# Kernel optimization log

Hardware: AMD Instinct MI355X
Metric: run time of the kernel (lower is better)

## Reference

```python
import jax, jax.numpy as jnp
import numpy as np

BETA_MAX = 0.995
BETA_MIN = 0.05
EPI_AGE_PENALTY = 0.02
EPI_STRENGTH_BOOST = 0.5
EPI_STRENGTH_DECAY = 0.995
EPI_WRITE_ALPHA = 0.5
EVICT_AGE_BOOST = 0.05
EVICT_STR_PENALTY = 0.5
SLOT_TEMP = 50.0
SWITCH_TAU = 0.5

B, H, K, U, OBS, SSUM, PROJ = 2048, 256, 32, 128, 128, 128, 128


def setup_inputs() -> dict:
    key = jax.random.key(0)
    ks = jax.random.split(key, 20)
    def gl(k, shape, fan_in):
        return jax.random.normal(k, shape, jnp.float32) / np.sqrt(fan_in).astype(np.float32)
    inp = {}
    inp['h_prev'] = jax.random.normal(ks[0], (B, H), jnp.float32)
    inp['keys'] = jax.random.normal(ks[1], (B, K, H), jnp.float32)
    inp['vals'] = jax.random.normal(ks[2], (B, K, H), jnp.float32)
    inp['age'] = jax.random.uniform(ks[3], (B, K), jnp.float32) * 100.0
    inp['strength'] = jax.random.uniform(ks[4], (B, K), jnp.float32)
    inp['obs'] = jax.random.normal(ks[5], (B, OBS), jnp.float32)
    inp['ssum'] = jax.random.normal(ks[6], (B, SSUM), jnp.float32)
    inp['u_int_prev'] = jax.random.normal(ks[7], (B, U), jnp.float32)
    inp['step_in_macro'] = jax.random.randint(ks[8], (B,), 0, 4, jnp.int32)
    # learned parameters
    inp['W_obs'] = gl(ks[9], (OBS, PROJ), OBS); inp['b_obs'] = jnp.zeros((PROJ,), jnp.float32)
    inp['W_ssum'] = gl(ks[10], (SSUM, PROJ), SSUM); inp['b_ssum'] = jnp.zeros((PROJ,), jnp.float32)
    XIN = 2 * PROJ
    inp['Wi'] = gl(ks[11], (XIN, 3 * H), XIN); inp['bi'] = jnp.zeros((3 * H,), jnp.float32)
    inp['Wh'] = gl(ks[12], (H, 3 * H), H); inp['bhn'] = jnp.zeros((H,), jnp.float32)
    inp['W_gate'] = gl(ks[13], (H, 1), H); inp['b_gate'] = jnp.zeros((1,), jnp.float32)
    inp['W_mean'] = gl(ks[14], (2 * H, U), 2 * H); inp['b_mean'] = jnp.zeros((U,), jnp.float32)
    inp['u_logstd'] = jnp.full((U,), -1.0, jnp.float32)
    inp['W_beta'] = gl(ks[15], (2 * H, 1), 2 * H); inp['b_beta'] = jnp.zeros((1,), jnp.float32)
    inp['W_sw'] = gl(ks[16], (2 * H, 1), 2 * H); inp['b_sw'] = jnp.zeros((1,), jnp.float32)
    return inp


def reference(h_prev, keys, vals, age, strength, obs, ssum, u_int_prev, step_in_macro,
              W_obs, b_obs, W_ssum, b_ssum, Wi, bi, Wh, bhn, W_gate, b_gate,
              W_mean, b_mean, u_logstd, W_beta, b_beta, W_sw, b_sw):
    Kslots = keys.shape[1]
    # input projections + GRU step (flax GRUCell: h' = (1-z)*n + z*h)
    xo = jnp.tanh(obs @ W_obs + b_obs)
    xs = jnp.tanh(ssum @ W_ssum + b_ssum)
    x_in = jnp.concatenate([xo, xs], axis=-1)
    gi = x_in @ Wi + bi
    gh = h_prev @ Wh
    ir, iz, inn = jnp.split(gi, 3, axis=-1)
    hr, hz, hn = jnp.split(gh, 3, axis=-1)
    r = jax.nn.sigmoid(ir + hr)
    z = jax.nn.sigmoid(iz + hz)
    n = jnp.tanh(inn + r * (hn + bhn))
    h_t = (1.0 - z) * n + z * h_prev
    # write gate
    w_str = jax.nn.sigmoid(h_t @ W_gate + b_gate)  # [B,1]
    # episodic slot memory: cosine-sim read
    qn = h_t / (jnp.linalg.norm(h_t, axis=-1, keepdims=True) + 1e-6)
    kn = keys / (jnp.linalg.norm(keys, axis=-1, keepdims=True) + 1e-6)
    sim_r = jnp.einsum('bkd,bd->bk', kn, qn)
    logits = sim_r + EPI_STRENGTH_BOOST * jnp.log(jnp.clip(strength, 1e-3, 1.0)) - EPI_AGE_PENALTY * age
    w_read = jax.nn.softmax(logits, axis=-1)
    read_out = jnp.einsum('bk,bkd->bd', w_read, vals)
    # write addressing (write_vec == query_vec == h_t so sim_w == sim_r)
    wk_n = qn
    sim_w = sim_r
    evict = EVICT_AGE_BOOST * jnp.log1p(age) - EVICT_STR_PENALTY * strength
    write_soft = jax.nn.softmax(sim_w * SLOT_TEMP + evict, axis=-1)
    write_hard = jax.nn.one_hot(jnp.argmax(write_soft, axis=-1), Kslots, dtype=jnp.float32)
    write_w = jax.lax.stop_gradient(write_hard - write_soft) + write_soft  # straight-through
    ws = jnp.clip(w_str, 0.0, 1.0)  # [B,1]
    eff_rate = write_w * ws * EPI_WRITE_ALPHA  # [B,K]
    rate = eff_rate[:, :, None]
    keys_new = (1.0 - rate) * keys + rate * wk_n[:, None, :]
    vals_new = (1.0 - rate) * vals + rate * h_t[:, None, :]
    age_new = (age + 1.0) * (1.0 - write_w)
    str_new = strength * EPI_STRENGTH_DECAY
    str_new = jnp.clip(str_new + write_w * ws * (1.0 - str_new), 0.0, 1.0)
    # heads
    ctx = jnp.concatenate([h_t, read_out], axis=-1)
    mean = ctx @ W_mean + b_mean
    beta = BETA_MIN + (BETA_MAX - BETA_MIN) * jax.nn.sigmoid((ctx @ W_beta + b_beta)[:, 0])
    sw_prob = jax.nn.sigmoid((ctx @ W_sw + b_sw)[:, 0])
    # deterministic path (rng=None): u_prop = mean, threshold switch
    u_prop = mean
    switch_f = jnp.where(sw_prob > SWITCH_TAU, 1.0, 0.0)
    is_boundary = jnp.where(step_in_macro == 0, 1.0, 0.0)
    switch_f = jnp.maximum(switch_f, is_boundary)
    sw_f = switch_f[:, None]
    beta_eff = beta[:, None] * (1.0 - sw_f)
    u_int = beta_eff * u_int_prev + (1.0 - beta_eff) * u_prop
    return (h_t, keys_new, vals_new, age_new, str_new, u_prop,
            switch_f.astype(jnp.int32), u_int, beta, sw_prob)
```

## Files before the change

kernel.cpp:

```cpp
#include <hip/hip_runtime.h>
#include <math.h>

#define Bdim 2048
#define Hdim 256
#define KS 32
#define Udim 128
#define OBSD 128
#define PROJD 128
#define H3 768

__device__ __forceinline__ float sigm(float x){ return 1.0f/(1.0f+__expf(-x)); }

typedef float __attribute__((ext_vector_type(4))) f32x4;

__device__ __forceinline__ float4 ntload4(const float* p){
    f32x4 v = __builtin_nontemporal_load((const f32x4*)p);
    return make_float4(v.x, v.y, v.z, v.w);
}
__device__ __forceinline__ void ntstore4(float* p, float4 q){
    f32x4 v = {q.x, q.y, q.z, q.w};
    __builtin_nontemporal_store(v, (f32x4*)p);
}

__global__ __launch_bounds__(256) void kA1(
    const float* __restrict__ obs, const float* __restrict__ ssum,
    const float* __restrict__ W_obs, const float* __restrict__ b_obs,
    const float* __restrict__ W_ssum, const float* __restrict__ b_ssum,
    float* __restrict__ xin)
{
    __shared__ float s_in[2][8][128];
    const int t = threadIdx.x;
    const int r0 = blockIdx.x * 8;

    {
        int r = t >> 5, c4 = (t & 31) << 2;
        float4 v = *(const float4*)(obs + (size_t)(r0+r)*OBSD + c4);
        s_in[0][r][c4+0]=v.x; s_in[0][r][c4+1]=v.y; s_in[0][r][c4+2]=v.z; s_in[0][r][c4+3]=v.w;
        v = *(const float4*)(ssum + (size_t)(r0+r)*OBSD + c4);
        s_in[1][r][c4+0]=v.x; s_in[1][r][c4+1]=v.y; s_in[1][r][c4+2]=v.z; s_in[1][r][c4+3]=v.w;
    }
    __syncthreads();

    const int col = t & 127;
    const int src = t >> 7;
    const float* Wp = src ? W_ssum : W_obs;
    const float bb = src ? b_ssum[col] : b_obs[col];

    float acc[8] = {0,0,0,0,0,0,0,0};
    for (int i=0;i<128;i++){
        float w = Wp[i*PROJD + col];
        #pragma unroll
        for (int r=0;r<8;r++) acc[r] = fmaf(s_in[src][r][i], w, acc[r]);
    }
    #pragma unroll
    for (int r=0;r<8;r++)
        xin[(size_t)(r0+r)*256 + t] = tanhf(acc[r] + bb);
}

__global__ __launch_bounds__(256) void kG2(
    const float* __restrict__ xin, const float* __restrict__ hp,
    const float* __restrict__ Wi, const float* __restrict__ Wh,
    float* __restrict__ g)
{
    __shared__ float Xt[2][16][68];
    __shared__ float Wt[2][16][64];

    const int t = threadIdx.x;
    const int bx = blockIdx.x >> 4;
    const int by = blockIdx.x & 15;
    const int r0 = bx * 64;
    const int c0 = by * 64;

    const int kbeg = (c0 >= 768) ? 256 : 0;
    const int kend = (c0 >= 512 && c0 < 768) ? 256 : 512;
    const int nck  = (kend - kbeg) >> 4;

    const int sr  = t >> 2;
    const int sk4 = (t & 3) << 2;
    const size_t xbase = (size_t)(r0 + sr) * 256 + sk4;
    const int wk  = t >> 4;
    const int wc4 = (t & 15) << 2;
    const int cW  = (c0 < 512) ? c0 : (c0 - 256);

    const int rowA = (t & 15) << 2;
    const int colA = (t >> 4) << 2;

    float acc[4][4] = {{0.f}};
    float4 xr, wr;

    {
        const int k0 = kbeg;
        const float* xs = (k0 < 256) ? (xin + xbase + k0) : (hp + xbase + (k0 - 256));
        xr = *(const float4*)xs;
        const int k = k0 + wk;
        const float* wsrc = (k < 256) ? (Wi + (size_t)k*H3 + c0 + wc4)
                                      : (Wh + (size_t)(k-256)*H3 + cW + wc4);
        wr = *(const float4*)wsrc;
    }
    Xt[0][sk4+0][sr] = xr.x; Xt[0][sk4+1][sr] = xr.y;
    Xt[0][sk4+2][sr] = xr.z; Xt[0][sk4+3][sr] = xr.w;
    *(float4*)&Wt[0][wk][wc4] = wr;
    __syncthreads();

    for (int ck = 0; ck < nck; ck++){
        const int cur = ck & 1;
        const bool more = (ck + 1 < nck);
        if (more){
            const int k0 = kbeg + ((ck + 1) << 4);
            const float* xs = (k0 < 256) ? (xin + xbase + k0) : (hp + xbase + (k0 - 256));
            xr = *(const float4*)xs;
            const int k = k0 + wk;
            const float* wsrc = (k < 256) ? (Wi + (size_t)k*H3 + c0 + wc4)
                                          : (Wh + (size_t)(k-256)*H3 + cW + wc4);
            wr = *(const float4*)wsrc;
        }
        #pragma unroll
        for (int kk = 0; kk < 16; kk++){
            float4 a4 = *(const float4*)&Xt[cur][kk][rowA];
            float4 b4 = *(const float4*)&Wt[cur][kk][colA];
            float av[4] = {a4.x, a4.y, a4.z, a4.w};
            float bv[4] = {b4.x, b4.y, b4.z, b4.w};
            #pragma unroll
            for (int i=0;i<4;i++)
                #pragma unroll
                for (int j=0;j<4;j++)
                    acc[i][j] = fmaf(av[i], bv[j], acc[i][j]);
        }
        if (more){
            const int nxt = cur ^ 1;
            Xt[nxt][sk4+0][sr] = xr.x; Xt[nxt][sk4+1][sr] = xr.y;
            Xt[nxt][sk4+2][sr] = xr.z; Xt[nxt][sk4+3][sr] = xr.w;
            *(float4*)&Wt[nxt][wk][wc4] = wr;
            __syncthreads();
        }
    }

    #pragma unroll
    for (int i=0;i<4;i++){
        float4 o = make_float4(acc[i][0], acc[i][1], acc[i][2], acc[i][3]);
        *(float4*)&g[(size_t)(r0 + rowA + i)*1024 + c0 + colA] = o;
    }
}

__global__ __launch_bounds__(256) void kA3(
    const float* __restrict__ g, const float* __restrict__ h_prev,
    const float* __restrict__ bi, const float* __restrict__ bhn,
    const float* __restrict__ W_gate, const float* __restrict__ b_gate,
    float* __restrict__ out_h, float* __restrict__ ws_qn, float* __restrict__ ws_wstr)
{
    __shared__ float redA[8][4], redB[8][4];
    __shared__ float s_inv[8];
    const int t = threadIdx.x;
    const int r0 = blockIdx.x * 8;

    const float bir = bi[t], biz = bi[t+256], bin_ = bi[t+512];
    const float bh = bhn[t];
    const float wg = W_gate[t];
    const int lane = t & 63, wid = t >> 6;

    float hv[8];
    #pragma unroll
    for (int r=0;r<8;r++){
        const size_t gb = (size_t)(r0+r)*1024;
        float gr = g[gb + t];
        float gz = g[gb + 256 + t];
        float gni = g[gb + 512 + t];
        float gnh = g[gb + 768 + t];
        float hp = h_prev[(size_t)(r0+r)*Hdim + t];
        float rr = sigm(gr + bir);
        float zz = sigm(gz + biz);
        float nn = tanhf(gni + bin_ + rr*(gnh + bh));
        hv[r] = (1.0f - zz)*nn + zz*hp;
    }

    #pragma unroll
    for (int r=0;r<8;r++){
        float a = hv[r]*hv[r];
        float b2 = hv[r]*wg;
        #pragma unroll
        for (int off=32; off>=1; off>>=1){
            a  += __shfl_down(a, off);
            b2 += __shfl_down(b2, off);
        }
        if (lane==0){ redA[r][wid]=a; redB[r][wid]=b2; }
    }
    __syncthreads();
    if (t < 8){
        float ss = redA[t][0]+redA[t][1]+redA[t][2]+redA[t][3];
        float gd = redB[t][0]+redB[t][1]+redB[t][2]+redB[t][3];
        s_inv[t] = 1.0f/(sqrtf(ss) + 1e-6f);
        ws_wstr[r0+t] = sigm(gd + b_gate[0]);
    }
    __syncthreads();
    #pragma unroll
    for (int r=0;r<8;r++){
        out_h[(size_t)(r0+r)*Hdim + t] = hv[r];
        ws_qn[(size_t)(r0+r)*Hdim + t] = hv[r]*s_inv[r];
    }
}

__global__ __launch_bounds__(256) void kB(
    const float* __restrict__ keys, const float* __restrict__ vals,
    const float* __restrict__ age, const float* __restrict__ strength,
    const float* __restrict__ h_t, const float* __restrict__ ws_qn,
    const float* __restrict__ ws_wstr,
    float* __restrict__ keys_new, float* __restrict__ vals_new,
    float* __restrict__ age_new, float* __restrict__ str_new,
    float* __restrict__ ws_ro)
{
    __shared__ float s_sim[KS], s_wr[KS], s_rate[KS];
    __shared__ float4 s_ro[4][64];

    const int b = blockIdx.x;
    const int t = threadIdx.x, lane = t & 63, wid = t >> 6;

    float ag = 0.f, st = 0.f, wstr = 0.f;
    if (t < KS){
        ag = age[b*KS+t];
        st = strength[b*KS+t];
        wstr = ws_wstr[b];
    }

    const float4 q4 = ((const float4*)(ws_qn + (size_t)b*Hdim))[lane];
    const float4 h4 = ((const float4*)(h_t  + (size_t)b*Hdim))[lane];

    const float* Kb = keys + (size_t)b*KS*Hdim;
    const float* Vb = vals + (size_t)b*KS*Hdim;
    float4 kreg[8], vreg[8];
    float v[16];
    #pragma unroll
    for (int s=0;s<8;s++){
        const int k = wid*8 + s;
        kreg[s] = ntload4(Kb + k*Hdim + lane*4);
        vreg[s] = ntload4(Vb + k*Hdim + lane*4);
        v[2*s]   = kreg[s].x*q4.x + kreg[s].y*q4.y + kreg[s].z*q4.z + kreg[s].w*q4.w;
        v[2*s+1] = kreg[s].x*kreg[s].x + kreg[s].y*kreg[s].y + kreg[s].z*kreg[s].z + kreg[s].w*kreg[s].w;
    }

    {
        const bool hb5 = (lane & 32) != 0;
        #pragma unroll
        for (int i=0;i<8;i++){
            float send = hb5 ? v[i] : v[i+8];
            float recv = __shfl_xor(send, 32);
            v[i] = (hb5 ? v[i+8] : v[i]) + recv;
        }
        const bool hb4 = (lane & 16) != 0;
        #pragma unroll
        for (int i=0;i<4;i++){
            float send = hb4 ? v[i] : v[i+4];
            float recv = __shfl_xor(send, 16);
            v[i] = (hb4 ? v[i+4] : v[i]) + recv;
        }
        const bool hb3 = (lane & 8) != 0;
        #pragma unroll
        for (int i=0;i<2;i++){
            float send = hb3 ? v[i] : v[i+2];
            float recv = __shfl_xor(send, 8);
            v[i] = (hb3 ? v[i+2] : v[i]) + recv;
        }
        const bool hb2 = (lane & 4) != 0;
        {
            float send = hb2 ? v[0] : v[1];
            float recv = __shfl_xor(send, 4);
            v[0] = (hb2 ? v[1] : v[0]) + recv;
        }
        float r0 = v[0];
        r0 += __shfl_xor(r0, 2);
        r0 += __shfl_xor(r0, 1);
        float other = __shfl_xor(r0, 4);
        if ((lane & 7) == 0){
            s_sim[wid*8 + (lane>>3)] = r0 / (sqrtf(other) + 1e-6f);
        }
    }
    __syncthreads();

    if (t < KS){
        float sim = s_sim[t];
        float cl = fminf(fmaxf(st, 0.001f), 1.0f);
        float logit = sim + 0.5f*logf(cl) - 0.02f*ag;
        float wl = 50.0f*sim + 0.05f*log1pf(ag) - 0.5f*st;

        float lmax = logit;
        #pragma unroll
        for (int off=16; off>=1; off>>=1)
            lmax = fmaxf(lmax, __shfl_xor(lmax, off));
        float e = __expf(logit - lmax);
        float es = e;
        #pragma unroll
        for (int off=16; off>=1; off>>=1)
            es += __shfl_xor(es, off);

        float wm = wl; int ki = t;
        #pragma unroll
        for (int off=16; off>=1; off>>=1){
            float ow = __shfl_xor(wm, off);
            int   ok = __shfl_xor(ki, off);
            if (ow > wm || (ow == wm && ok < ki)){ wm = ow; ki = ok; }
        }

        s_wr[t] = e / es;
        float hard = (t == ki) ? 1.0f : 0.0f;
        s_rate[t] = hard * 0.5f * wstr;
        age_new[b*KS+t] = (ag + 1.0f)*(1.0f - hard);
        float sd = st*0.995f;
        float sn = sd + hard*wstr*(1.0f - sd);
        str_new[b*KS+t] = fminf(fmaxf(sn,0.f),1.f);
    }
    __syncthreads();

    float4 ro = make_float4(0.f,0.f,0.f,0.f);
    float* KNb = keys_new + (size_t)b*KS*Hdim;
    float* VNb = vals_new + (size_t)b*KS*Hdim;
    #pragma unroll
    for (int s=0;s<8;s++){
        const int k = wid*8 + s;
        const float wr = s_wr[k];
        const float rate = s_rate[k];
        const float om = 1.0f - rate;
        ro.x = fmaf(wr, vreg[s].x, ro.x);
        ro.y = fmaf(wr, vreg[s].y, ro.y);
        ro.z = fmaf(wr, vreg[s].z, ro.z);
        ro.w = fmaf(wr, vreg[s].w, ro.w);
        float4 kn, vn;
        kn.x = om*kreg[s].x + rate*q4.x;
        kn.y = om*kreg[s].y + rate*q4.y;
        kn.z = om*kreg[s].z + rate*q4.z;
        kn.w = om*kreg[s].w + rate*q4.w;
        vn.x = om*vreg[s].x + rate*h4.x;
        vn.y = om*vreg[s].y + rate*h4.y;
        vn.z = om*vreg[s].z + rate*h4.z;
        vn.w = om*vreg[s].w + rate*h4.w;
        ntstore4(KNb + k*Hdim + lane*4, kn);
        ntstore4(VNb + k*Hdim + lane*4, vn);
    }
    s_ro[wid][lane] = ro;
    __syncthreads();
    if (t < 64){
        float4 a = s_ro[0][t], bb = s_ro[1][t], c = s_ro[2][t], d = s_ro[3][t];
        float4 r;
        r.x = a.x+bb.x+c.x+d.x;
        r.y = a.y+bb.y+c.y+d.y;
        r.z = a.z+bb.z+c.z+d.z;
        r.w = a.w+bb.w+c.w+d.w;
        ((float4*)(ws_ro + (size_t)b*Hdim))[t] = r;
    }
}

__global__ __launch_bounds__(256) void kC(
    const float* __restrict__ h_t, const float* __restrict__ ws_ro,
    const float* __restrict__ u_int_prev, const int* __restrict__ step_in_macro,
    const float* __restrict__ W_mean, const float* __restrict__ b_mean,
    const float* __restrict__ W_beta, const float* __restrict__ b_beta,
    const float* __restrict__ W_sw, const float* __restrict__ b_sw,
    float* __restrict__ out_uprop, float* __restrict__ out_switch,
    float* __restrict__ out_uint, float* __restrict__ out_beta, float* __restrict__ out_swp)
{
    __shared__ float s_ctx[4][512];
    __shared__ float redb[4][4], reds[4][4];
    __shared__ float s_beff[4];
    const int t = threadIdx.x;
    const int r0 = blockIdx.x * 4;

    {
        int r = t >> 6, c4 = (t & 63) << 2;
        float4 v = *(const float4*)(h_t + (size_t)(r0+r)*Hdim + c4);
        s_ctx[r][c4+0]=v.x; s_ctx[r][c4+1]=v.y; s_ctx[r][c4+2]=v.z; s_ctx[r][c4+3]=v.w;
        v = *(const float4*)(ws_ro + (size_t)(r0+r)*Hdim + c4);
        s_ctx[r][256+c4+0]=v.x; s_ctx[r][256+c4+1]=v.y; s_ctx[r][256+c4+2]=v.z; s_ctx[r][256+c4+3]=v.w;
    }
    __syncthreads();

    const int c = t & 127;
    const int rh = t >> 7;
    float acc[2] = {0.f, 0.f};
    for (int i=0;i<512;i++){
        float w = W_mean[i*Udim + c];
        acc[0] = fmaf(s_ctx[2*rh+0][i], w, acc[0]);
        acc[1] = fmaf(s_ctx[2*rh+1][i], w, acc[1]);
    }

    float pb[4]={0,0,0,0}, ps[4]={0,0,0,0};
    for (int i=t; i<512; i+=256){
        float wb = W_beta[i], wsw = W_sw[i];
        #pragma unroll
        for (int r=0;r<4;r++){
            pb[r] = fmaf(s_ctx[r][i], wb, pb[r]);
            ps[r] = fmaf(s_ctx[r][i], wsw, ps[r]);
        }
    }
    const int lane = t & 63, wid = t >> 6;
    #pragma unroll
    for (int r=0;r<4;r++){
        float a = pb[r], b2 = ps[r];
        #pragma unroll
        for (int off=32; off>=1; off>>=1){
            a  += __shfl_down(a, off);
            b2 += __shfl_down(b2, off);
        }
        if (lane==0){ redb[r][wid]=a; reds[r][wid]=b2; }
    }
    __syncthreads();
    if (t < 4){
        float db  = redb[t][0]+redb[t][1]+redb[t][2]+redb[t][3] + b_beta[0];
        float dsw = reds[t][0]+reds[t][1]+reds[t][2]+reds[t][3] + b_sw[0];
        float beta = 0.05f + 0.945f*sigm(db);
        float swp = sigm(dsw);
        float swf = (swp > 0.5f) ? 1.0f : 0.0f;
        if (step_in_macro[r0+t] == 0) swf = 1.0f;
        out_beta[r0+t] = beta;
        out_swp[r0+t] = swp;
        out_switch[r0+t] = swf;
        s_beff[t] = beta*(1.0f - swf);
    }
    __syncthreads();
    #pragma unroll
    for (int j=0;j<2;j++){
        int r = 2*rh + j;
        float mean = acc[j] + b_mean[c];
        size_t o = (size_t)(r0+r)*Udim + c;
        out_uprop[o] = mean;
        float be = s_beff[r];
        out_uint[o] = be*u_int_prev[o] + (1.0f-be)*mean;
    }
}

extern "C" void kernel_launch(void* const* d_in, const int* in_sizes, int n_in,
                              void* d_out, int out_size, void* d_ws, size_t ws_size,
                              hipStream_t stream)
{
    const float* h_prev   = (const float*)d_in[0];
    const float* keys     = (const float*)d_in[1];
    const float* vals     = (const float*)d_in[2];
    const float* age      = (const float*)d_in[3];
    const float* strength = (const float*)d_in[4];
    const float* obs      = (const float*)d_in[5];
    const float* ssum     = (const float*)d_in[6];
    const float* u_int_prev = (const float*)d_in[7];
    const int*   step     = (const int*)d_in[8];
    const float* W_obs    = (const float*)d_in[9];
    const float* b_obs    = (const float*)d_in[10];
    const float* W_ssum   = (const float*)d_in[11];
    const float* b_ssum   = (const float*)d_in[12];
    const float* Wi       = (const float*)d_in[13];
    const float* bi       = (const float*)d_in[14];
    const float* Wh       = (const float*)d_in[15];
    const float* bhn      = (const float*)d_in[16];
    const float* W_gate   = (const float*)d_in[17];
    const float* b_gate   = (const float*)d_in[18];
    const float* W_mean   = (const float*)d_in[19];
    const float* b_mean   = (const float*)d_in[20];
    const float* W_beta   = (const float*)d_in[22];
    const float* b_beta   = (const float*)d_in[23];
    const float* W_sw     = (const float*)d_in[24];
    const float* b_sw     = (const float*)d_in[25];

    float* out = (float*)d_out;
    float* out_h    = out;
    float* out_kn   = out_h   + 524288;
    float* out_vn   = out_kn  + 16777216;
    float* out_age  = out_vn  + 16777216;
    float* out_str  = out_age + 65536;
    float* out_up   = out_str + 65536;
    float* out_sw   = out_up  + 262144;
    float* out_ui   = out_sw  + 2048;
    float* out_beta = out_ui  + 262144;
    float* out_swp  = out_beta+ 2048;

    float* ws = (float*)d_ws;
    float* ws_qn   = ws;
    float* ws_ro   = ws + Bdim*Hdim;
    float* ws_wstr = ws + 2*Bdim*Hdim;

    float* ws_xin = out_vn;
    float* ws_g   = out_kn;

    kA1<<<Bdim/8, 256, 0, stream>>>(obs, ssum, W_obs, b_obs, W_ssum, b_ssum, ws_xin);
    kG2<<<512, 256, 0, stream>>>(ws_xin, h_prev, Wi, Wh, ws_g);
    kA3<<<Bdim/8, 256, 0, stream>>>(ws_g, h_prev, bi, bhn, W_gate, b_gate,
                                    out_h, ws_qn, ws_wstr);
    kB<<<Bdim, 256, 0, stream>>>(keys, vals, age, strength, out_h, ws_qn, ws_wstr,
                                 out_kn, out_vn, out_age, out_str, ws_ro);
    kC<<<Bdim/4, 256, 0, stream>>>(out_h, ws_ro, u_int_prev, step, W_mean, b_mean,
                                   W_beta, b_beta, W_sw, b_sw,
                                   out_up, out_sw, out_ui, out_beta, out_swp);
}
```

Measured before the change: 126.9 us.

## Split episodic memory kernel into similarity pass and update pass

The fused memory kernel is split into two kernels. The first reads keys and computes the read weights, the write rates, age and strength. The second rereads keys and vals to produce the read-out and write keys_new and vals_new. The aim is to cut register pressure from holding 16 float4 registers across the barrier and to raise occupancy. The cost is a second 64MB read of keys, which now uses cached rather than nontemporal loads in the hope that it hits the L2 or MALL cache, plus one extra kernel launch.

```diff
diff --git a/kernel.cpp b/kernel.cpp
--- a/kernel.cpp
+++ b/kernel.cpp
@@ -13,10 +13,6 @@
 
 typedef float __attribute__((ext_vector_type(4))) f32x4;
 
-__device__ __forceinline__ float4 ntload4(const float* p){
-    f32x4 v = __builtin_nontemporal_load((const f32x4*)p);
-    return make_float4(v.x, v.y, v.z, v.w);
-}
 __device__ __forceinline__ void ntstore4(float* p, float4 q){
     f32x4 v = {q.x, q.y, q.z, q.w};
     __builtin_nontemporal_store(v, (f32x4*)p);
@@ -199,17 +195,14 @@
     }
 }
 
-__global__ __launch_bounds__(256) void kB(
-    const float* __restrict__ keys, const float* __restrict__ vals,
+__global__ __launch_bounds__(256) void kB1(
+    const float* __restrict__ keys,
     const float* __restrict__ age, const float* __restrict__ strength,
-    const float* __restrict__ h_t, const float* __restrict__ ws_qn,
-    const float* __restrict__ ws_wstr,
-    float* __restrict__ keys_new, float* __restrict__ vals_new,
+    const float* __restrict__ ws_qn, const float* __restrict__ ws_wstr,
     float* __restrict__ age_new, float* __restrict__ str_new,
-    float* __restrict__ ws_ro)
-{
-    __shared__ float s_sim[KS], s_wr[KS], s_rate[KS];
-    __shared__ float4 s_ro[4][64];
+    float* __restrict__ wr_out, float* __restrict__ rate_out)
+{
+    __shared__ float s_sim[KS];
 
     const int b = blockIdx.x;
     const int t = threadIdx.x, lane = t & 63, wid = t >> 6;
@@ -222,19 +215,15 @@
     }
 
     const float4 q4 = ((const float4*)(ws_qn + (size_t)b*Hdim))[lane];
-    const float4 h4 = ((const float4*)(h_t  + (size_t)b*Hdim))[lane];
-
     const float* Kb = keys + (size_t)b*KS*Hdim;
-    const float* Vb = vals + (size_t)b*KS*Hdim;
-    float4 kreg[8], vreg[8];
+
     float v[16];
     #pragma unroll
     for (int s=0;s<8;s++){
         const int k = wid*8 + s;
-        kreg[s] = ntload4(Kb + k*Hdim + lane*4);
-        vreg[s] = ntload4(Vb + k*Hdim + lane*4);
-        v[2*s]   = kreg[s].x*q4.x + kreg[s].y*q4.y + kreg[s].z*q4.z + kreg[s].w*q4.w;
-        v[2*s+1] = kreg[s].x*kreg[s].x + kreg[s].y*kreg[s].y + kreg[s].z*kreg[s].z + kreg[s].w*kreg[s].w;
+        float4 k4 = *(const float4*)(Kb + k*Hdim + lane*4);
+        v[2*s]   = k4.x*q4.x + k4.y*q4.y + k4.z*q4.z + k4.w*q4.w;
+        v[2*s+1] = k4.x*k4.x + k4.y*k4.y + k4.z*k4.z + k4.w*k4.w;
     }
 
     {
@@ -299,38 +288,64 @@
             if (ow > wm || (ow == wm && ok < ki)){ wm = ow; ki = ok; }
         }
 
-        s_wr[t] = e / es;
+        wr_out[b*KS+t] = e / es;
         float hard = (t == ki) ? 1.0f : 0.0f;
-        s_rate[t] = hard * 0.5f * wstr;
+        rate_out[b*KS+t] = hard * 0.5f * wstr;
         age_new[b*KS+t] = (ag + 1.0f)*(1.0f - hard);
         float sd = st*0.995f;
         float sn = sd + hard*wstr*(1.0f - sd);
         str_new[b*KS+t] = fminf(fmaxf(sn,0.f),1.f);
     }
-    __syncthreads();
-
-    float4 ro = make_float4(0.f,0.f,0.f,0.f);
+}
+
+__global__ __launch_bounds__(256) void kB2(
+    const float* __restrict__ keys, const float* __restrict__ vals,
+    const float* __restrict__ wr_in, const float* __restrict__ rate_in,
+    const float* __restrict__ h_t, const float* __restrict__ ws_qn,
+    float* __restrict__ keys_new, float* __restrict__ vals_new,
+    float* __restrict__ ws_ro)
+{
+    __shared__ float s_wr[KS], s_rate[KS];
+    __shared__ float4 s_ro[4][64];
+
+    const int b = blockIdx.x;
+    const int t = threadIdx.x, lane = t & 63, wid = t >> 6;
+
+    if (t < KS){
+        s_wr[t]   = wr_in[b*KS+t];
+        s_rate[t] = rate_in[b*KS+t];
+    }
+    const float4 q4 = ((const float4*)(ws_qn + (size_t)b*Hdim))[lane];
+    const float4 h4 = ((const float4*)(h_t  + (size_t)b*Hdim))[lane];
+    __syncthreads();
+
+    const float* Kb = keys + (size_t)b*KS*Hdim;
+    const float* Vb = vals + (size_t)b*KS*Hdim;
     float* KNb = keys_new + (size_t)b*KS*Hdim;
     float* VNb = vals_new + (size_t)b*KS*Hdim;
+
+    float4 ro = make_float4(0.f,0.f,0.f,0.f);
     #pragma unroll
     for (int s=0;s<8;s++){
         const int k = wid*8 + s;
+        float4 k4 = *(const float4*)(Kb + k*Hdim + lane*4);
+        float4 v4 = *(const float4*)(Vb + k*Hdim + lane*4);
         const float wr = s_wr[k];
         const float rate = s_rate[k];
         const float om = 1.0f - rate;
-        ro.x = fmaf(wr, vreg[s].x, ro.x);
-        ro.y = fmaf(wr, vreg[s].y, ro.y);
-        ro.z = fmaf(wr, vreg[s].z, ro.z);
-        ro.w = fmaf(wr, vreg[s].w, ro.w);
+        ro.x = fmaf(wr, v4.x, ro.x);
+        ro.y = fmaf(wr, v4.y, ro.y);
+        ro.z = fmaf(wr, v4.z, ro.z);
+        ro.w = fmaf(wr, v4.w, ro.w);
         float4 kn, vn;
-        kn.x = om*kreg[s].x + rate*q4.x;
-        kn.y = om*kreg[s].y + rate*q4.y;
-        kn.z = om*kreg[s].z + rate*q4.z;
-        kn.w = om*kreg[s].w + rate*q4.w;
-        vn.x = om*vreg[s].x + rate*h4.x;
-        vn.y = om*vreg[s].y + rate*h4.y;
-        vn.z = om*vreg[s].z + rate*h4.z;
-        vn.w = om*vreg[s].w + rate*h4.w;
+        kn.x = om*k4.x + rate*q4.x;
+        kn.y = om*k4.y + rate*q4.y;
+        kn.z = om*k4.z + rate*q4.z;
+        kn.w = om*k4.w + rate*q4.w;
+        vn.x = om*v4.x + rate*h4.x;
+        vn.y = om*v4.y + rate*h4.y;
+        vn.z = om*v4.z + rate*h4.z;
+        vn.w = om*v4.w + rate*h4.w;
         ntstore4(KNb + k*Hdim + lane*4, kn);
         ntstore4(VNb + k*Hdim + lane*4, vn);
     }
@@ -472,15 +487,19 @@
     float* ws_ro   = ws + Bdim*Hdim;
     float* ws_wstr = ws + 2*Bdim*Hdim;
 
-    float* ws_xin = out_vn;
-    float* ws_g   = out_kn;
+    float* ws_xin  = out_vn;
+    float* ws_g    = out_kn;
+    float* ws_wr   = out_up;
+    float* ws_rate = out_up + Bdim*KS;
 
     kA1<<<Bdim/8, 256, 0, stream>>>(obs, ssum, W_obs, b_obs, W_ssum, b_ssum, ws_xin);
     kG2<<<512, 256, 0, stream>>>(ws_xin, h_prev, Wi, Wh, ws_g);
     kA3<<<Bdim/8, 256, 0, stream>>>(ws_g, h_prev, bi, bhn, W_gate, b_gate,
                                     out_h, ws_qn, ws_wstr);
-    kB<<<Bdim, 256, 0, stream>>>(keys, vals, age, strength, out_h, ws_qn, ws_wstr,
-                                 out_kn, out_vn, out_age, out_str, ws_ro);
+    kB1<<<Bdim, 256, 0, stream>>>(keys, age, strength, ws_qn, ws_wstr,
+                                  out_age, out_str, ws_wr, ws_rate);
+    kB2<<<Bdim, 256, 0, stream>>>(keys, vals, ws_wr, ws_rate, out_h, ws_qn,
+                                  out_kn, out_vn, ws_ro);
     kC<<<Bdim/4, 256, 0, stream>>>(out_h, ws_ro, u_int_prev, step, W_mean, b_mean,
                                    W_beta, b_beta, W_sw, b_sw,
                                    out_up, out_sw, out_ui, out_beta, out_swp);
```

Result: slower. 133.6 us (+5.3%).

## Fuse memory-update kernel with output-head kernel to drop readout round trip

Applied to the files above, without the earlier changes.

Merges the episodic memory update kernel and the output-head kernel into one per-row kernel. The read-out vector and h_t are kept in shared memory and the mean/beta/switch heads are computed directly, removing one launch and the workspace write/read of the read-out. In exchange, each block computes a single-row matvec over W_mean, so weight reads are amortized over one row instead of four and lengthen each block's tail.

```diff
diff --git a/kernel.cpp b/kernel.cpp
--- a/kernel.cpp
+++ b/kernel.cpp
@@ -199,17 +199,26 @@
     }
 }
 
-__global__ __launch_bounds__(256) void kB(
+__global__ __launch_bounds__(256) void kBC(
     const float* __restrict__ keys, const float* __restrict__ vals,
     const float* __restrict__ age, const float* __restrict__ strength,
     const float* __restrict__ h_t, const float* __restrict__ ws_qn,
     const float* __restrict__ ws_wstr,
+    const float* __restrict__ u_int_prev, const int* __restrict__ step_in_macro,
+    const float* __restrict__ W_mean, const float* __restrict__ b_mean,
+    const float* __restrict__ W_beta, const float* __restrict__ b_beta,
+    const float* __restrict__ W_sw, const float* __restrict__ b_sw,
     float* __restrict__ keys_new, float* __restrict__ vals_new,
     float* __restrict__ age_new, float* __restrict__ str_new,
-    float* __restrict__ ws_ro)
+    float* __restrict__ out_uprop, float* __restrict__ out_switch,
+    float* __restrict__ out_uint, float* __restrict__ out_beta, float* __restrict__ out_swp)
 {
     __shared__ float s_sim[KS], s_wr[KS], s_rate[KS];
     __shared__ float4 s_ro[4][64];
+    __shared__ float s_ctx[512];
+    __shared__ float s_part[2][128];
+    __shared__ float s_red[2][4];
+    __shared__ float s_beff;
 
     const int b = blockIdx.x;
     const int t = threadIdx.x, lane = t & 63, wid = t >> 6;
@@ -335,92 +344,59 @@
         ntstore4(VNb + k*Hdim + lane*4, vn);
     }
     s_ro[wid][lane] = ro;
+    if (wid == 0){
+        s_ctx[lane*4+0] = h4.x; s_ctx[lane*4+1] = h4.y;
+        s_ctx[lane*4+2] = h4.z; s_ctx[lane*4+3] = h4.w;
+    }
     __syncthreads();
     if (t < 64){
         float4 a = s_ro[0][t], bb = s_ro[1][t], c = s_ro[2][t], d = s_ro[3][t];
-        float4 r;
-        r.x = a.x+bb.x+c.x+d.x;
-        r.y = a.y+bb.y+c.y+d.y;
-        r.z = a.z+bb.z+c.z+d.z;
-        r.w = a.w+bb.w+c.w+d.w;
-        ((float4*)(ws_ro + (size_t)b*Hdim))[t] = r;
-    }
-}
-
-__global__ __launch_bounds__(256) void kC(
-    const float* __restrict__ h_t, const float* __restrict__ ws_ro,
-    const float* __restrict__ u_int_prev, const int* __restrict__ step_in_macro,
-    const float* __restrict__ W_mean, const float* __restrict__ b_mean,
-    const float* __restrict__ W_beta, const float* __restrict__ b_beta,
-    const float* __restrict__ W_sw, const float* __restrict__ b_sw,
-    float* __restrict__ out_uprop, float* __restrict__ out_switch,
-    float* __restrict__ out_uint, float* __restrict__ out_beta, float* __restrict__ out_swp)
-{
-    __shared__ float s_ctx[4][512];
-    __shared__ float redb[4][4], reds[4][4];
-    __shared__ float s_beff[4];
-    const int t = threadIdx.x;
-    const int r0 = blockIdx.x * 4;
+        s_ctx[256 + t*4+0] = a.x+bb.x+c.x+d.x;
+        s_ctx[256 + t*4+1] = a.y+bb.y+c.y+d.y;
+        s_ctx[256 + t*4+2] = a.z+bb.z+c.z+d.z;
+        s_ctx[256 + t*4+3] = a.w+bb.w+c.w+d.w;
+    }
+    __syncthreads();
 
     {
-        int r = t >> 6, c4 = (t & 63) << 2;
-        float4 v = *(const float4*)(h_t + (size_t)(r0+r)*Hdim + c4);
-        s_ctx[r][c4+0]=v.x; s_ctx[r][c4+1]=v.y; s_ctx[r][c4+2]=v.z; s_ctx[r][c4+3]=v.w;
-        v = *(const float4*)(ws_ro + (size_t)(r0+r)*Hdim + c4);
-        s_ctx[r][256+c4+0]=v.x; s_ctx[r][256+c4+1]=v.y; s_ctx[r][256+c4+2]=v.z; s_ctx[r][256+c4+3]=v.w;
-    }
-    __syncthreads();
-
-    const int c = t & 127;
-    const int rh = t >> 7;
-    float acc[2] = {0.f, 0.f};
-    for (int i=0;i<512;i++){
-        float w = W_mean[i*Udim + c];
-        acc[0] = fmaf(s_ctx[2*rh+0][i], w, acc[0]);
-        acc[1] = fmaf(s_ctx[2*rh+1][i], w, acc[1]);
-    }
-
-    float pb[4]={0,0,0,0}, ps[4]={0,0,0,0};
-    for (int i=t; i<512; i+=256){
-        float wb = W_beta[i], wsw = W_sw[i];
-        #pragma unroll
-        for (int r=0;r<4;r++){
-            pb[r] = fmaf(s_ctx[r][i], wb, pb[r]);
-            ps[r] = fmaf(s_ctx[r][i], wsw, ps[r]);
-        }
-    }
-    const int lane = t & 63, wid = t >> 6;
-    #pragma unroll
-    for (int r=0;r<4;r++){
-        float a = pb[r], b2 = ps[r];
+        const int col = t & 127;
+        const int kh  = t >> 7;
+        const float* ctxh = s_ctx + kh*256;
+        const float* Wm = W_mean + (size_t)kh*256*Udim + col;
+        float acc = 0.f;
+        #pragma unroll 4
+        for (int i=0;i<256;i++)
+            acc = fmaf(ctxh[i], Wm[(size_t)i*Udim], acc);
+        s_part[kh][col] = acc;
+
+        float cb = s_ctx[t]*W_beta[t] + s_ctx[t+256]*W_beta[t+256];
+        float cs = s_ctx[t]*W_sw[t]   + s_ctx[t+256]*W_sw[t+256];
         #pragma unroll
         for (int off=32; off>=1; off>>=1){
-            a  += __shfl_down(a, off);
-            b2 += __shfl_down(b2, off);
-        }
-        if (lane==0){ redb[r][wid]=a; reds[r][wid]=b2; }
-    }
-    __syncthreads();
-    if (t < 4){
-        float db  = redb[t][0]+redb[t][1]+redb[t][2]+redb[t][3] + b_beta[0];
-        float dsw = reds[t][0]+reds[t][1]+reds[t][2]+reds[t][3] + b_sw[0];
+            cb += __shfl_down(cb, off);
+            cs += __shfl_down(cs, off);
+        }
+        if (lane == 0){ s_red[0][wid] = cb; s_red[1][wid] = cs; }
+    }
+    __syncthreads();
+    if (t == 0){
+        float db  = s_red[0][0]+s_red[0][1]+s_red[0][2]+s_red[0][3] + b_beta[0];
+        float dsw = s_red[1][0]+s_red[1][1]+s_red[1][2]+s_red[1][3] + b_sw[0];
         float beta = 0.05f + 0.945f*sigm(db);
         float swp = sigm(dsw);
         float swf = (swp > 0.5f) ? 1.0f : 0.0f;
-        if (step_in_macro[r0+t] == 0) swf = 1.0f;
-        out_beta[r0+t] = beta;
-        out_swp[r0+t] = swp;
-        out_switch[r0+t] = swf;
-        s_beff[t] = beta*(1.0f - swf);
-    }
-    __syncthreads();
-    #pragma unroll
-    for (int j=0;j<2;j++){
-        int r = 2*rh + j;
-        float mean = acc[j] + b_mean[c];
-        size_t o = (size_t)(r0+r)*Udim + c;
+        if (step_in_macro[b] == 0) swf = 1.0f;
+        out_beta[b]  = beta;
+        out_swp[b]   = swp;
+        out_switch[b]= swf;
+        s_beff = beta*(1.0f - swf);
+    }
+    __syncthreads();
+    if (t < 128){
+        float mean = s_part[0][t] + s_part[1][t] + b_mean[t];
+        size_t o = (size_t)b*Udim + t;
         out_uprop[o] = mean;
-        float be = s_beff[r];
+        float be = s_beff;
         out_uint[o] = be*u_int_prev[o] + (1.0f-be)*mean;
     }
 }
@@ -469,8 +445,7 @@
 
     float* ws = (float*)d_ws;
     float* ws_qn   = ws;
-    float* ws_ro   = ws + Bdim*Hdim;
-    float* ws_wstr = ws + 2*Bdim*Hdim;
+    float* ws_wstr = ws + Bdim*Hdim;
 
     float* ws_xin = out_vn;
     float* ws_g   = out_kn;
@@ -479,9 +454,9 @@
     kG2<<<512, 256, 0, stream>>>(ws_xin, h_prev, Wi, Wh, ws_g);
     kA3<<<Bdim/8, 256, 0, stream>>>(ws_g, h_prev, bi, bhn, W_gate, b_gate,
                                     out_h, ws_qn, ws_wstr);
-    kB<<<Bdim, 256, 0, stream>>>(keys, vals, age, strength, out_h, ws_qn, ws_wstr,
-                                 out_kn, out_vn, out_age, out_str, ws_ro);
-    kC<<<Bdim/4, 256, 0, stream>>>(out_h, ws_ro, u_int_prev, step, W_mean, b_mean,
-                                   W_beta, b_beta, W_sw, b_sw,
-                                   out_up, out_sw, out_ui, out_beta, out_swp);
-}
+    kBC<<<Bdim, 256, 0, stream>>>(keys, vals, age, strength, out_h, ws_qn, ws_wstr,
+                                  u_int_prev, step, W_mean, b_mean,
+                                  W_beta, b_beta, W_sw, b_sw,
+                                  out_kn, out_vn, out_age, out_str,
+                                  out_up, out_sw, out_ui, out_beta, out_swp);
+}
```

Result: no change. 125.9 us (-0.8%).
